# Optimization experiments

Hardware: AMD Instinct MI355X
Metric: run time of the kernel (lower is better)

The kernel has to match this reference:

```python
import jax, jax.numpy as jnp
import numpy as np

PROJ_EPS = 4e-3      # geoopt-style Poincare projection margin (float32)
MIN_NORM = 1e-15
ATANH_EPS = 1e-5     # clamp arg of arctanh away from 1
WEI_EPS = 1e-3       # self.eps buffer
P_EXP = 2.0          # self.p buffer


def _project(v, k):
    # Project onto Poincare ball of curvature -k: clip norm to (1-eps)/sqrt(k).
    # k has shape (1,H,1,1), v has shape (B,H,T,D).
    maxnorm = (1.0 - PROJ_EPS) / jnp.sqrt(k)
    norm = jnp.sqrt(jnp.clip(jnp.sum(v * v, axis=-1, keepdims=True), MIN_NORM))
    return jnp.where(norm > maxnorm, v / norm * maxnorm, v)


def setup_inputs() -> dict:
    key = jax.random.key(0)
    k1, k2, k3, k4 = jax.random.split(key, 4)
    B, T, C, H = 4, 1024, 768, 12
    x = jax.random.normal(k1, (B, T, C), dtype=jnp.float32)
    Wqkv = jax.random.normal(k2, (3 * C, C), dtype=jnp.float32) * (1.0 / np.sqrt(C))
    Wproj = jax.random.normal(k3, (C, C), dtype=jnp.float32) * (1.0 / np.sqrt(C))
    # learnable per-head curvature, init ~ exp(randn)*curvature (must be > 0)
    kcurv = jax.random.uniform(k4, (1, H, 1, 1), dtype=jnp.float32, minval=0.5, maxval=1.5)
    return {"x": x, "Wqkv": Wqkv, "Wproj": Wproj, "kcurv": kcurv}


def reference(x, Wqkv, Wproj, kcurv):
    B, T, C = x.shape
    H = kcurv.shape[1]
    D = C // H

    qkv = x @ Wqkv.T                                  # (B,T,3C)
    q, kx, v = jnp.split(qkv, 3, axis=-1)

    def to_heads(t):
        return t.reshape(B, T, H, D).transpose(0, 2, 1, 3)  # (B,H,T,D)

    q, kx, v = to_heads(q), to_heads(kx), to_heads(v)

    qp = _project(q, kcurv)
    kp = _project(kx, kcurv)

    # Poincare distance d(x,y) = (2/sqrt(k)) * artanh(sqrt(k)*||(-x) mobius+ y||).
    # mobius_add(-x,y) = (-(1-2k<x,y>+k|y|^2) x + (1-k|x|^2) y) / (1-2k<x,y>+k^2|x|^2|y|^2)
    # => ||num||^2 = A^2|x|^2 + Bc^2|y|^2 - 2*A*Bc*<x,y>, avoiding (B,H,T,T,D) tensors.
    x2 = jnp.sum(qp * qp, axis=-1)                    # (B,H,T)
    y2 = jnp.sum(kp * kp, axis=-1)                    # (B,H,T)
    xy = jnp.einsum('bhid,bhjd->bhij', qp, kp)        # (B,H,T,T)

    kc = kcurv                                        # (1,H,1,1) broadcasts to (B,H,T,T)
    x2i = x2[..., :, None]                            # (B,H,T,1)
    y2j = y2[..., None, :]                            # (B,H,1,T)

    A = 1.0 - 2.0 * kc * xy + kc * y2j
    Bc = 1.0 - kc * x2i
    num2 = A * A * x2i + Bc * Bc * y2j - 2.0 * A * Bc * xy
    denom = 1.0 - 2.0 * kc * xy + (kc * kc) * x2i * y2j
    madd_norm = jnp.sqrt(jnp.clip(num2, MIN_NORM)) / jnp.clip(denom, MIN_NORM)

    sk = jnp.sqrt(kc)
    dist = (2.0 / sk) * jnp.arctanh(jnp.clip(sk * madd_norm, 0.0, 1.0 - ATANH_EPS))

    wei = 1.0 / (WEI_EPS + dist ** P_EXP)             # (B,H,T,T)
    causal = jnp.tril(jnp.ones((T, T), dtype=bool))
    wei = jnp.where(causal, wei, 0.0)
    wei = wei / jnp.sum(wei, axis=-1, keepdims=True)

    y = jnp.einsum('bhij,bhjd->bhid', wei, v)         # (B,H,T,D)
    y = y.transpose(0, 2, 1, 3).reshape(B, T, C)
    return y @ Wproj.T
```

## Files before the change

### kernel.cpp

```cpp
#include <hip/hip_runtime.h>
#include <hip/hip_bf16.h>
#include <math.h>

#define PROJ_EPSF 0.004f
#define MIN_NORMF 1e-15f
#define ATANH_EPSF 1e-5f
#define WEI_EPSF 1e-3f
#define LN2F 0.69314718055994531f

#define TT 1024
#define CC 768
#define HH 12
#define BBATCH 4

typedef unsigned long long ull;
typedef __attribute__((ext_vector_type(4))) float f32x4;
typedef __attribute__((ext_vector_type(8))) short bf16x8;

#define MFMA(a, b, c) __builtin_amdgcn_mfma_f32_16x16x32_bf16(a, b, c, 0, 0, 0)

static __device__ __forceinline__ uint cvtpk(float a, float b) {
    uint r;
    asm("v_cvt_pk_bf16_f32 %0, %1, %2" : "=v"(r) : "v"(a), "v"(b));
    return r;
}
static __device__ __forceinline__ ushort f2bf(float f) {
    uint u = __float_as_uint(f);
    u += 0x7fffu + ((u >> 16) & 1u);
    return (ushort)(u >> 16);
}
static __device__ __forceinline__ float bf2f(ushort h) {
    return __uint_as_float(((uint)h) << 16);
}
static __device__ __forceinline__ void split4(const float4& f, ull& hp, ull& lp) {
    uint h01 = cvtpk(f.x, f.y), h23 = cvtpk(f.z, f.w);
    float r0 = f.x - __uint_as_float(h01 << 16);
    float r1 = f.y - __uint_as_float(h01 & 0xffff0000u);
    float r2 = f.z - __uint_as_float(h23 << 16);
    float r3 = f.w - __uint_as_float(h23 & 0xffff0000u);
    uint l01 = cvtpk(r0, r1), l23 = cvtpk(r2, r3);
    hp = ((ull)h23 << 32) | h01;
    lp = ((ull)l23 << 32) | l01;
}
union pk16 { bf16x8 v; ull u[2]; };
static __device__ __forceinline__ void gl_lds16(const void* g, void* l) {
    __builtin_amdgcn_global_load_lds(
        (const __attribute__((address_space(1))) unsigned int*)g,
        (__attribute__((address_space(3))) unsigned int*)l, 16, 0, 0);
}

__global__ __launch_bounds__(256) void wprep(const float* __restrict__ W,
                                             ushort* __restrict__ Wh,
                                             ushort* __restrict__ Wl, int n4) {
    int i = blockIdx.x * 256 + threadIdx.x;
    if (i < n4) {
        float4 f = ((const float4*)W)[i];
        ull hp, lp;
        split4(f, hp, lp);
        ((ull*)Wh)[i] = hp;
        ((ull*)Wl)[i] = lp;
    }
}

__global__ __launch_bounds__(256) void gemm_qkv(
        const float* __restrict__ x, const ushort* __restrict__ Wh,
        const ushort* __restrict__ Wl, const float* __restrict__ kcurv,
        ushort* __restrict__ qh, ushort* __restrict__ ql,
        ushort* __restrict__ kh, ushort* __restrict__ kl,
        ushort* __restrict__ vT, float* __restrict__ x2g,
        float* __restrict__ y2g) {
    __shared__ ushort Ah[2][64 * 64], Al[2][64 * 64], Bh[2][64 * 64], Bl[2][64 * 64];
    const int tid = threadIdx.x, lane = tid & 63, wv = tid >> 6;
    const int wr = wv >> 1, wc = wv & 1, lr = lane & 15, lg = lane >> 4;
    const int m0 = blockIdx.x * 128, n0 = blockIdx.y * 128;
    const bool isV = (n0 >= 2 * CC);

    const int arow = tid >> 1, akh = tid & 1;
    const float* Ap = x + (size_t)(m0 + arow) * CC + akh * 16;
    const int ap_ = arow >> 1;
    const int ag0 = 4 * (arow & 1) + 2 * akh;
    const int aoff0 = ap_ * 128 + ((ag0 ^ (ap_ & 7)) << 4);
    const int aoff1 = ap_ * 128 + (((ag0 + 1) ^ (ap_ & 7)) << 4);
    const int c0 = 2 * wv, c1 = 2 * wv + 1;
    const int p0 = 8 * c0 + (lane >> 3), q0 = (lane & 7) ^ (p0 & 7);
    const int p1 = 8 * c1 + (lane >> 3), q1 = (lane & 7) ^ (p1 & 7);
    const size_t bs0 = (size_t)(n0 + 2 * p0 + (q0 >> 2)) * CC + (q0 & 3) * 8;
    const size_t bs1 = (size_t)(n0 + 2 * p1 + (q1 >> 2)) * CC + (q1 & 3) * 8;
    const int goff = (((4 * (lr & 1) + lg) ^ ((lr >> 1) & 7)) << 4);
    const int pa = wr * 32 + (lr >> 1);
    const int pb = wc * 32 + (lr >> 1);

    f32x4 acc[4][4] = {};
    float4 av[4];

#define STAGE_B(BUF, KK)                                                          \
    gl_lds16(Wh + bs0 + (KK), (char*)Bh[BUF] + c0 * 1024);                        \
    gl_lds16(Wh + bs1 + (KK), (char*)Bh[BUF] + c1 * 1024);                        \
    if (!isV) {                                                                   \
        gl_lds16(Wl + bs0 + (KK), (char*)Bl[BUF] + c0 * 1024);                    \
        gl_lds16(Wl + bs1 + (KK), (char*)Bl[BUF] + c1 * 1024);                    \
    }
#define SPLIT_A(BUF)                                                              \
    {                                                                             \
        pk16 h_, l_;                                                              \
        split4(av[0], h_.u[0], l_.u[0]);                                          \
        split4(av[1], h_.u[1], l_.u[1]);                                          \
        *(bf16x8*)((char*)Ah[BUF] + aoff0) = h_.v;                                \
        if (!isV) *(bf16x8*)((char*)Al[BUF] + aoff0) = l_.v;                      \
        split4(av[2], h_.u[0], l_.u[0]);                                          \
        split4(av[3], h_.u[1], l_.u[1]);                                          \
        *(bf16x8*)((char*)Ah[BUF] + aoff1) = h_.v;                                \
        if (!isV) *(bf16x8*)((char*)Al[BUF] + aoff1) = l_.v;                      \
    }
#define LOAD_A(KK)                                                                \
    { _Pragma("unroll") for (int q = 0; q < 4; ++q)                               \
        av[q] = *(const float4*)(Ap + (KK) + 4 * q); }

    LOAD_A(0)
    STAGE_B(0, 0)
    SPLIT_A(0)
    LOAD_A(32)
    asm volatile("s_waitcnt vmcnt(4) lgkmcnt(0)" ::: "memory");
    __builtin_amdgcn_s_barrier();
    __builtin_amdgcn_sched_barrier(0);

    int cur = 0;
    for (int kk = 0; kk < CC; kk += 32) {
        const bool notLast = (kk + 32 < CC);
        if (notLast) {
            STAGE_B(cur ^ 1, kk + 32)
            SPLIT_A(cur ^ 1)
            if (kk + 64 < CC) LOAD_A(kk + 64)
            __builtin_amdgcn_sched_barrier(0);
        }
        if (!isV) {
            bf16x8 a_h[4], a_l[4];
#pragma unroll
            for (int m = 0; m < 4; ++m) {
                const int off = (pa + m * 8) * 128 + goff;
                a_h[m] = *(const bf16x8*)((char*)Ah[cur] + off);
                a_l[m] = *(const bf16x8*)((char*)Al[cur] + off);
            }
#pragma unroll
            for (int n = 0; n < 4; ++n) {
                const int off = (pb + n * 8) * 128 + goff;
                bf16x8 b_h = *(const bf16x8*)((char*)Bh[cur] + off);
                bf16x8 b_l = *(const bf16x8*)((char*)Bl[cur] + off);
#pragma unroll
                for (int m = 0; m < 4; ++m) {
                    acc[m][n] = MFMA(a_h[m], b_h, acc[m][n]);
                    acc[m][n] = MFMA(a_h[m], b_l, acc[m][n]);
                    acc[m][n] = MFMA(a_l[m], b_h, acc[m][n]);
                }
            }
        } else {
            bf16x8 a_h[4], b_h[4];
#pragma unroll
            for (int m = 0; m < 4; ++m)
                a_h[m] = *(const bf16x8*)((char*)Ah[cur] + (pa + m * 8) * 128 + goff);
#pragma unroll
            for (int n = 0; n < 4; ++n)
                b_h[n] = *(const bf16x8*)((char*)Bh[cur] + (pb + n * 8) * 128 + goff);
#pragma unroll
            for (int n = 0; n < 4; ++n)
#pragma unroll
                for (int m = 0; m < 4; ++m)
                    acc[n][m] = MFMA(b_h[n], a_h[m], acc[n][m]);
        }
        if (notLast) {
            if (kk + 64 < CC)
                asm volatile("s_waitcnt vmcnt(4) lgkmcnt(0)" ::: "memory");
            else
                asm volatile("s_waitcnt vmcnt(0) lgkmcnt(0)" ::: "memory");
            __builtin_amdgcn_s_barrier();
            __builtin_amdgcn_sched_barrier(0);
        }
        cur ^= 1;
    }
#undef STAGE_B
#undef SPLIT_A
#undef LOAD_A

    if (isV) {
        const int hd = (n0 - 2 * CC) / 64 + wc;
#pragma unroll
        for (int n = 0; n < 4; ++n)
#pragma unroll
            for (int m = 0; m < 4; ++m)
#pragma unroll
                for (int r = 0; r < 4; ++r) {
                    const int dl = n * 16 + lg * 4 + r;
                    const int tok = m0 + wr * 64 + m * 16 + lr;
                    vT[(size_t)(hd * 64 + dl) * 4096 + tok] = f2bf(acc[n][m][r]);
                }
    } else {
        const bool isQ = (n0 < CC);
        const int hd = (isQ ? n0 : n0 - CC) / 64 + wc;
        ushort* ph = isQ ? qh : kh;
        ushort* pl = isQ ? ql : kl;
        float* sg = isQ ? x2g : y2g;
        const float kcv = kcurv[hd];
        const float mxn = (1.0f - PROJ_EPSF) / sqrtf(kcv);
        const float mxn2 = mxn * mxn;
#pragma unroll
        for (int m = 0; m < 4; ++m)
#pragma unroll
            for (int r = 0; r < 4; ++r) {
                float s = 0.f;
#pragma unroll
                for (int n = 0; n < 4; ++n) s = fmaf(acc[m][n][r], acc[m][n][r], s);
                s += __shfl_xor(s, 1);
                s += __shfl_xor(s, 2);
                s += __shfl_xor(s, 4);
                s += __shfl_xor(s, 8);
                float scale = 1.0f, x2v = s;
                if (s > mxn2) {
                    scale = mxn * __builtin_amdgcn_rcpf(sqrtf(s));
                    x2v = s * scale * scale;
                }
                const int tok = m0 + wr * 64 + m * 16 + lg * 4 + r;
                const size_t rowb = (size_t)tok * CC + (isQ ? n0 : n0 - CC) + wc * 64;
#pragma unroll
                for (int n = 0; n < 4; ++n) {
                    const float v = acc[m][n][r] * scale;
                    const ushort hb = f2bf(v);
                    ph[rowb + n * 16 + lr] = hb;
                    pl[rowb + n * 16 + lr] = f2bf(v - bf2f(hb));
                }
                if (lr == 0)
                    sg[(size_t)((tok >> 10) * HH + hd) * TT + (tok & 1023)] = x2v;
            }
    }
}

__global__ __launch_bounds__(256) void hyp_attn(
        const ushort* __restrict__ qh, const ushort* __restrict__ ql,
        const ushort* __restrict__ kh, const ushort* __restrict__ kl,
        const ushort* __restrict__ vT, const float* __restrict__ x2g,
        const float* __restrict__ y2g, const float* __restrict__ kcurv,
        ushort* __restrict__ yh, ushort* __restrict__ yl) {
    const int ib = (int)blockIdx.x;
    const int xcd = ib & 7, t = ib >> 3;
    const int tcr = t / 6;
    const int which = t - tcr * 6;
    const int g64 = 15 - tcr;
    const int bh = which * 8 + xcd;
    const int b = bh / HH, h = bh - b * HH;
    const int tid = threadIdx.x, lane = tid & 63, wv = tid >> 6;
    const int lr = lane & 15, lg = lane >> 4;
    const int rg = g64 * 4 + wv;
    const int rgq = g64;

    __shared__ char ldsK[2][16384];
    __shared__ char ldsV[8192];
    __shared__ ushort wtb[4][16 * 72];
    ushort* wtw = wtb[wv];

    const float kc = kcurv[h];
    const float sk = sqrtf(kc);
    const float distc = LN2F / sk;
    const float d2c = distc * distc;
    const float twokc = 2.0f * kc;
    const float cA = 1.0f - ATANH_EPSF;

    const size_t qrb = (size_t)(b * TT + rg * 16 + lr) * CC + h * 64 + lg * 8;
    const bf16x8 qH0 = *(const bf16x8*)(qh + qrb), qH1 = *(const bf16x8*)(qh + qrb + 32);
    const bf16x8 qL0 = *(const bf16x8*)(ql + qrb), qL1 = *(const bf16x8*)(ql + qrb + 32);
    const float4 x2v = *(const float4*)&x2g[(size_t)bh * TT + rg * 16 + lg * 4];
    const float x2a[4] = { x2v.x, x2v.y, x2v.z, x2v.w };
    float kx2[4], Bc[4], Bc2[4];
#pragma unroll
    for (int r = 0; r < 4; ++r) {
        kx2[r] = kc * x2a[r];
        Bc[r] = 1.0f - kx2[r];
        Bc2[r] = Bc[r] * Bc[r];
    }

    const int srow8 = lane >> 3;
    const int sgrp = (lane & 7) ^ (srow8 & 7);
    const int so0 = ((lg ^ (lr & 7)) << 4);
    const int so1 = (((4 + lg) ^ (lr & 7)) << 4);
    const int lro = lr << 7;

#define STAGE_K(BUF, J0)                                                          \
    { _Pragma("unroll") for (int c4 = 0; c4 < 2; ++c4) {                          \
        const int c = wv * 2 + c4;                                                \
        const size_t gsrc = (size_t)(b * TT + (J0) + c * 8 + srow8) * CC + h * 64 + sgrp * 8; \
        gl_lds16(kh + gsrc, (char*)(BUF) + c * 1024);                             \
        gl_lds16(kl + gsrc, (char*)(BUF) + 8192 + c * 1024);                      \
    } }
#define STAGE_V(J0)                                                               \
    { _Pragma("unroll") for (int c4 = 0; c4 < 2; ++c4) {                          \
        const int c = wv * 2 + c4;                                                \
        gl_lds16(vT + (size_t)(h * 64 + c * 8 + srow8) * 4096 + b * TT + (J0) + sgrp * 8, \
                 ldsV + c * 1024);                                                \
    } }

#define TRANSF(NN, SA, Y2R)                                                        \
    {                                                                              \
        const float ky2 = kc * (Y2R);                                              \
        const float p1 = 1.0f + ky2;                                               \
        const int jg = j0 + NN * 16 + lr;                                          \
        _Pragma("unroll") for (int r = 0; r < 4; ++r) {                            \
            const float xy = SA[r];                                                \
            const float t2 = twokc * xy;                                           \
            const float Aa = p1 - t2;                                              \
            const float dn = fmaxf(fmaf(kx2[r], ky2, 1.0f) - t2, MIN_NORMF);       \
            const float ABxy = Aa * (Bc[r] * xy);                                  \
            const float c1 = fmaf(Bc2[r], (Y2R), -2.0f * ABxy);                    \
            const float num2 = fmaf(Aa * Aa, x2a[r], c1);                          \
            const float s = sqrtf(fmaxf(num2, MIN_NORMF));                         \
            const float sm = fminf(sk * s, cA * dn);                               \
            const float L = __builtin_amdgcn_logf((dn + sm) *                      \
                                __builtin_amdgcn_rcpf(dn - sm));                   \
            float w = __builtin_amdgcn_rcpf(fmaf(L * L, d2c, WEI_EPSF));           \
            if (mk && (jg > rg * 16 + lg * 4 + r)) w = 0.0f;                       \
            wtw[(lg * 4 + r) * 72 + NN * 16 + lr] = f2bf(w);                       \
            wsum[r] += w;                                                          \
        }                                                                          \
    }

    f32x4 pv[4] = {};
    float wsum[4] = {};

    STAGE_K(ldsK[0], 0)

    int cur = 0;
    for (int jt = 0; jt <= rgq; ++jt) {
        const int j0 = jt * 64;
        const bool mk = (jt == rgq);
        STAGE_V(j0)
        if (jt < rgq) {
            STAGE_K(ldsK[cur ^ 1], j0 + 64)
            asm volatile("s_waitcnt vmcnt(6)" ::: "memory");
        } else {
            asm volatile("s_waitcnt vmcnt(2)" ::: "memory");
        }
        __builtin_amdgcn_s_barrier();
        __builtin_amdgcn_sched_barrier(0);
        const size_t y2b = (size_t)bh * TT + j0 + lr;
        const float y2n[4] = { y2g[y2b], y2g[y2b + 16], y2g[y2b + 32], y2g[y2b + 48] };
        __builtin_amdgcn_s_setprio(1);
        f32x4 sacc[4] = {};
#pragma unroll
        for (int n = 0; n < 4; ++n) {
            const char* p = ldsK[cur] + n * 2048 + lro;
            bf16x8 h0 = *(const bf16x8*)(p + so0);
            bf16x8 h1 = *(const bf16x8*)(p + so1);
            bf16x8 l0 = *(const bf16x8*)(p + 8192 + so0);
            bf16x8 l1 = *(const bf16x8*)(p + 8192 + so1);
            sacc[n] = MFMA(qH0, h0, sacc[n]);
            sacc[n] = MFMA(qH0, l0, sacc[n]);
            sacc[n] = MFMA(qL0, h0, sacc[n]);
            sacc[n] = MFMA(qH1, h1, sacc[n]);
            sacc[n] = MFMA(qH1, l1, sacc[n]);
            sacc[n] = MFMA(qL1, h1, sacc[n]);
        }
        TRANSF(0, sacc[0], y2n[0])
        TRANSF(1, sacc[1], y2n[1])
        TRANSF(2, sacc[2], y2n[2])
        TRANSF(3, sacc[3], y2n[3])
        __builtin_amdgcn_s_setprio(0);
        if (jt < rgq)
            asm volatile("s_waitcnt vmcnt(4)" ::: "memory");
        else
            asm volatile("s_waitcnt vmcnt(0)" ::: "memory");
        __builtin_amdgcn_s_barrier();
        __builtin_amdgcn_sched_barrier(0);
        __builtin_amdgcn_s_setprio(1);
        bf16x8 pw0 = *(const bf16x8*)&wtw[lr * 72 + lg * 8];
        bf16x8 pw1 = *(const bf16x8*)&wtw[lr * 72 + 32 + lg * 8];
#pragma unroll
        for (int n = 0; n < 4; ++n) {
            const char* p = ldsV + n * 2048 + lro;
            bf16x8 v0 = *(const bf16x8*)(p + so0);
            bf16x8 v1 = *(const bf16x8*)(p + so1);
            pv[n] = MFMA(pw0, v0, pv[n]);
            pv[n] = MFMA(pw1, v1, pv[n]);
        }
        __builtin_amdgcn_s_setprio(0);
        __builtin_amdgcn_s_barrier();
        cur ^= 1;
    }

    float den[4];
#pragma unroll
    for (int r = 0; r < 4; ++r) {
        float s = wsum[r];
        s += __shfl_xor(s, 1);
        s += __shfl_xor(s, 2);
        s += __shfl_xor(s, 4);
        s += __shfl_xor(s, 8);
        den[r] = s;
    }
#pragma unroll
    for (int r = 0; r < 4; ++r) {
        const float iv = __builtin_amdgcn_rcpf(den[r]);
        const size_t rowb = (size_t)(b * TT + rg * 16 + lg * 4 + r) * CC + h * 64;
#pragma unroll
        for (int n = 0; n < 4; ++n) {
            const float val = pv[n][r] * iv;
            const ushort hb = f2bf(val);
            yh[rowb + n * 16 + lr] = hb;
            yl[rowb + n * 16 + lr] = f2bf(val - bf2f(hb));
        }
    }
#undef TRANSF
#undef STAGE_K
#undef STAGE_V
}

__global__ __launch_bounds__(256) void gemm_out(const ushort* __restrict__ Ahp,
                                                const ushort* __restrict__ Alp,
                                                const ushort* __restrict__ Wh,
                                                const ushort* __restrict__ Wl,
                                                float* __restrict__ C) {
    __shared__ ushort Ah[2][32 * 64], Al[2][32 * 64], Bh[2][32 * 64], Bl[2][32 * 64];
    const int tid = threadIdx.x, lane = tid & 63, wv = tid >> 6;
    const int wr = wv >> 1, wc = wv & 1, lr = lane & 15, lg = lane >> 4;
    const int m0 = blockIdx.x * 64, n0 = blockIdx.y * 64;

    const int sp = 8 * wv + (lane >> 3);
    const int sg = (lane & 7) ^ (sp & 7);
    const int srow = 2 * sp + (sg >> 2);
    const int scol = (sg & 3) * 8;
    const size_t asrc = (size_t)(m0 + srow) * CC + scol;
    const size_t bsrc = (size_t)(n0 + srow) * CC + scol;
    const int goff = (((4 * (lr & 1) + lg) ^ ((lr >> 1) & 7)) << 4);
    const int pa = wr * 16 + (lr >> 1);
    const int pb = wc * 16 + (lr >> 1);

    f32x4 acc[2][2] = {};

#define STAGE_O(BUF, KK)                                                          \
    gl_lds16(Ahp + asrc + (KK), (char*)Ah[BUF] + wv * 1024);                      \
    gl_lds16(Alp + asrc + (KK), (char*)Al[BUF] + wv * 1024);                      \
    gl_lds16(Wh + bsrc + (KK), (char*)Bh[BUF] + wv * 1024);                       \
    gl_lds16(Wl + bsrc + (KK), (char*)Bl[BUF] + wv * 1024);

    STAGE_O(0, 0)
    int cur = 0;
    for (int kk = 0; kk < CC; kk += 32) {
        if (kk + 32 < CC) {
            STAGE_O(cur ^ 1, kk + 32)
            asm volatile("s_waitcnt vmcnt(4)" ::: "memory");
        } else {
            asm volatile("s_waitcnt vmcnt(0)" ::: "memory");
        }
        __builtin_amdgcn_s_barrier();
        __builtin_amdgcn_sched_barrier(0);
        bf16x8 a_h[2], a_l[2];
#pragma unroll
        for (int m = 0; m < 2; ++m) {
            const int off = (pa + m * 8) * 128 + goff;
            a_h[m] = *(const bf16x8*)((char*)Ah[cur] + off);
            a_l[m] = *(const bf16x8*)((char*)Al[cur] + off);
        }
#pragma unroll
        for (int n = 0; n < 2; ++n) {
            const int off = (pb + n * 8) * 128 + goff;
            bf16x8 b_h = *(const bf16x8*)((char*)Bh[cur] + off);
            bf16x8 b_l = *(const bf16x8*)((char*)Bl[cur] + off);
#pragma unroll
            for (int m = 0; m < 2; ++m) {
                acc[m][n] = MFMA(a_h[m], b_h, acc[m][n]);
                acc[m][n] = MFMA(a_h[m], b_l, acc[m][n]);
                acc[m][n] = MFMA(a_l[m], b_h, acc[m][n]);
            }
        }
        __builtin_amdgcn_s_barrier();
        cur ^= 1;
    }
#undef STAGE_O
#pragma unroll
    for (int m = 0; m < 2; ++m)
#pragma unroll
        for (int n = 0; n < 2; ++n)
#pragma unroll
            for (int r = 0; r < 4; ++r)
                C[(size_t)(m0 + wr * 32 + m * 16 + lg * 4 + r) * CC + n0 + wc * 32 + n * 16 + lr] =
                    acc[m][n][r];
}

extern "C" void kernel_launch(void* const* d_in, const int* in_sizes, int n_in,
                              void* d_out, int out_size, void* d_ws, size_t ws_size,
                              hipStream_t stream) {
    const float* x     = (const float*)d_in[0];
    const float* Wqkv  = (const float*)d_in[1];
    const float* Wproj = (const float*)d_in[2];
    const float* kcurv = (const float*)d_in[3];
    float* out = (float*)d_out;

    const size_t PL = (size_t)4096 * CC;
    char* w = (char*)d_ws;
    ushort* Wqh = (ushort*)w;
    ushort* Wql = Wqh + (size_t)2304 * CC;
    ushort* yh  = (ushort*)w;
    ushort* yl  = yh + PL;
    ushort* qh  = (ushort*)(w + 2 * PL * 2);
    ushort* ql  = qh + PL;
    ushort* kh  = ql + PL;
    ushort* kl  = kh + PL;
    ushort* vT  = kl + PL;
    ushort* Wph = vT + PL;
    ushort* Wpl = Wph + (size_t)CC * CC;
    float* x2g  = (float*)(Wpl + (size_t)CC * CC);
    float* y2g  = x2g + 48 * TT;

    wprep<<<2304 * CC / 4 / 256, 256, 0, stream>>>(Wqkv, Wqh, Wql, 2304 * CC / 4);
    wprep<<<CC * CC / 4 / 256, 256, 0, stream>>>(Wproj, Wph, Wpl, CC * CC / 4);
    gemm_qkv<<<dim3(32, 18), 256, 0, stream>>>(x, Wqh, Wql, kcurv,
                                               qh, ql, kh, kl, vT, x2g, y2g);
    hyp_attn<<<768, 256, 0, stream>>>(qh, ql, kh, kl, vT, x2g, y2g, kcurv, yh, yl);
    gemm_out<<<dim3(64, 12), 256, 0, stream>>>(yh, yl, Wph, Wpl, out);
}
```

Baseline: 142.7 us.

## Widen attention blocks to 128 query rows and merge weight-prep launches

The attention kernel now runs 8 waves per block covering 128 query rows, so each staged K/V tile is shared by twice as many waves and each wave issues half as many global-to-LDS loads. Waves whose causal range has ended sit idle but still join the barriers until the block's last tile. The two weight-split launches are merged into one kernel. The aim is to cut K/V staging traffic and launch overhead, at the cost of causal imbalance inside blocks and lower per-block parallelism.

Measured after the change: 150.9 us. 5.8% more time.

```diff
diff --git a/kernel.cpp b/kernel.cpp
--- a/kernel.cpp
+++ b/kernel.cpp
@@ -49,16 +49,28 @@
         (__attribute__((address_space(3))) unsigned int*)l, 16, 0, 0);
 }
 
-__global__ __launch_bounds__(256) void wprep(const float* __restrict__ W,
-                                             ushort* __restrict__ Wh,
-                                             ushort* __restrict__ Wl, int n4) {
+__global__ __launch_bounds__(256) void wprep2(const float* __restrict__ Wq,
+                                              const float* __restrict__ Wp,
+                                              ushort* __restrict__ Wqh,
+                                              ushort* __restrict__ Wql,
+                                              ushort* __restrict__ Wph,
+                                              ushort* __restrict__ Wpl) {
+    const int n1 = 2304 * CC / 4;
+    const int n2 = CC * CC / 4;
     int i = blockIdx.x * 256 + threadIdx.x;
-    if (i < n4) {
-        float4 f = ((const float4*)W)[i];
+    if (i < n1) {
+        float4 f = ((const float4*)Wq)[i];
         ull hp, lp;
         split4(f, hp, lp);
-        ((ull*)Wh)[i] = hp;
-        ((ull*)Wl)[i] = lp;
+        ((ull*)Wqh)[i] = hp;
+        ((ull*)Wql)[i] = lp;
+    } else if (i < n1 + n2) {
+        int j = i - n1;
+        float4 f = ((const float4*)Wp)[j];
+        ull hp, lp;
+        split4(f, hp, lp);
+        ((ull*)Wph)[j] = hp;
+        ((ull*)Wpl)[j] = lp;
     }
 }
 
@@ -233,7 +245,7 @@
     }
 }
 
-__global__ __launch_bounds__(256) void hyp_attn(
+__global__ __launch_bounds__(512) void hyp_attn(
         const ushort* __restrict__ qh, const ushort* __restrict__ ql,
         const ushort* __restrict__ kh, const ushort* __restrict__ kl,
         const ushort* __restrict__ vT, const float* __restrict__ x2g,
@@ -241,19 +253,19 @@
         ushort* __restrict__ yh, ushort* __restrict__ yl) {
     const int ib = (int)blockIdx.x;
     const int xcd = ib & 7, t = ib >> 3;
-    const int tcr = t / 6;
-    const int which = t - tcr * 6;
-    const int g64 = 15 - tcr;
+    const int g128 = 7 - t / 6;
+    const int which = t % 6;
     const int bh = which * 8 + xcd;
     const int b = bh / HH, h = bh - b * HH;
     const int tid = threadIdx.x, lane = tid & 63, wv = tid >> 6;
     const int lr = lane & 15, lg = lane >> 4;
-    const int rg = g64 * 4 + wv;
-    const int rgq = g64;
+    const int rg = g128 * 8 + wv;
+    const int rgq = rg >> 2;
+    const int rgqMax = 2 * g128 + 1;
 
     __shared__ char ldsK[2][16384];
     __shared__ char ldsV[8192];
-    __shared__ ushort wtb[4][16 * 72];
+    __shared__ ushort wtb[8][16 * 72];
     ushort* wtw = wtb[wv];
 
     const float kc = kcurv[h];
@@ -283,18 +295,14 @@
     const int lro = lr << 7;
 
 #define STAGE_K(BUF, J0)                                                          \
-    { _Pragma("unroll") for (int c4 = 0; c4 < 2; ++c4) {                          \
-        const int c = wv * 2 + c4;                                                \
-        const size_t gsrc = (size_t)(b * TT + (J0) + c * 8 + srow8) * CC + h * 64 + sgrp * 8; \
-        gl_lds16(kh + gsrc, (char*)(BUF) + c * 1024);                             \
-        gl_lds16(kl + gsrc, (char*)(BUF) + 8192 + c * 1024);                      \
-    } }
+    {                                                                             \
+        const size_t gsrc = (size_t)(b * TT + (J0) + wv * 8 + srow8) * CC + h * 64 + sgrp * 8; \
+        gl_lds16(kh + gsrc, (char*)(BUF) + wv * 1024);                            \
+        gl_lds16(kl + gsrc, (char*)(BUF) + 8192 + wv * 1024);                     \
+    }
 #define STAGE_V(J0)                                                               \
-    { _Pragma("unroll") for (int c4 = 0; c4 < 2; ++c4) {                          \
-        const int c = wv * 2 + c4;                                                \
-        gl_lds16(vT + (size_t)(h * 64 + c * 8 + srow8) * 4096 + b * TT + (J0) + sgrp * 8, \
-                 ldsV + c * 1024);                                                \
-    } }
+    gl_lds16(vT + (size_t)(h * 64 + wv * 8 + srow8) * 4096 + b * TT + (J0) + sgrp * 8, \
+             ldsV + wv * 1024);
 
 #define TRANSF(NN, SA, Y2R)                                                        \
     {                                                                              \
@@ -326,59 +334,64 @@
     STAGE_K(ldsK[0], 0)
 
     int cur = 0;
-    for (int jt = 0; jt <= rgq; ++jt) {
+    for (int jt = 0; jt <= rgqMax; ++jt) {
         const int j0 = jt * 64;
+        const bool active = (jt <= rgq);
         const bool mk = (jt == rgq);
         STAGE_V(j0)
-        if (jt < rgq) {
+        if (jt < rgqMax) {
             STAGE_K(ldsK[cur ^ 1], j0 + 64)
-            asm volatile("s_waitcnt vmcnt(6)" ::: "memory");
+            asm volatile("s_waitcnt vmcnt(3)" ::: "memory");
         } else {
-            asm volatile("s_waitcnt vmcnt(2)" ::: "memory");
+            asm volatile("s_waitcnt vmcnt(1)" ::: "memory");
         }
         __builtin_amdgcn_s_barrier();
         __builtin_amdgcn_sched_barrier(0);
-        const size_t y2b = (size_t)bh * TT + j0 + lr;
-        const float y2n[4] = { y2g[y2b], y2g[y2b + 16], y2g[y2b + 32], y2g[y2b + 48] };
-        __builtin_amdgcn_s_setprio(1);
-        f32x4 sacc[4] = {};
-#pragma unroll
-        for (int n = 0; n < 4; ++n) {
-            const char* p = ldsK[cur] + n * 2048 + lro;
-            bf16x8 h0 = *(const bf16x8*)(p + so0);
-            bf16x8 h1 = *(const bf16x8*)(p + so1);
-            bf16x8 l0 = *(const bf16x8*)(p + 8192 + so0);
-            bf16x8 l1 = *(const bf16x8*)(p + 8192 + so1);
-            sacc[n] = MFMA(qH0, h0, sacc[n]);
-            sacc[n] = MFMA(qH0, l0, sacc[n]);
-            sacc[n] = MFMA(qL0, h0, sacc[n]);
-            sacc[n] = MFMA(qH1, h1, sacc[n]);
-            sacc[n] = MFMA(qH1, l1, sacc[n]);
-            sacc[n] = MFMA(qL1, h1, sacc[n]);
-        }
-        TRANSF(0, sacc[0], y2n[0])
-        TRANSF(1, sacc[1], y2n[1])
-        TRANSF(2, sacc[2], y2n[2])
-        TRANSF(3, sacc[3], y2n[3])
-        __builtin_amdgcn_s_setprio(0);
-        if (jt < rgq)
-            asm volatile("s_waitcnt vmcnt(4)" ::: "memory");
+        if (active) {
+            const size_t y2b = (size_t)bh * TT + j0 + lr;
+            const float y2n[4] = { y2g[y2b], y2g[y2b + 16], y2g[y2b + 32], y2g[y2b + 48] };
+            __builtin_amdgcn_s_setprio(1);
+            f32x4 sacc[4] = {};
+#pragma unroll
+            for (int n = 0; n < 4; ++n) {
+                const char* p = ldsK[cur] + n * 2048 + lro;
+                bf16x8 h0 = *(const bf16x8*)(p + so0);
+                bf16x8 h1 = *(const bf16x8*)(p + so1);
+                bf16x8 l0 = *(const bf16x8*)(p + 8192 + so0);
+                bf16x8 l1 = *(const bf16x8*)(p + 8192 + so1);
+                sacc[n] = MFMA(qH0, h0, sacc[n]);
+                sacc[n] = MFMA(qH0, l0, sacc[n]);
+                sacc[n] = MFMA(qL0, h0, sacc[n]);
+                sacc[n] = MFMA(qH1, h1, sacc[n]);
+                sacc[n] = MFMA(qH1, l1, sacc[n]);
+                sacc[n] = MFMA(qL1, h1, sacc[n]);
+            }
+            TRANSF(0, sacc[0], y2n[0])
+            TRANSF(1, sacc[1], y2n[1])
+            TRANSF(2, sacc[2], y2n[2])
+            TRANSF(3, sacc[3], y2n[3])
+            __builtin_amdgcn_s_setprio(0);
+        }
+        if (jt < rgqMax)
+            asm volatile("s_waitcnt vmcnt(2)" ::: "memory");
         else
             asm volatile("s_waitcnt vmcnt(0)" ::: "memory");
         __builtin_amdgcn_s_barrier();
         __builtin_amdgcn_sched_barrier(0);
-        __builtin_amdgcn_s_setprio(1);
-        bf16x8 pw0 = *(const bf16x8*)&wtw[lr * 72 + lg * 8];
-        bf16x8 pw1 = *(const bf16x8*)&wtw[lr * 72 + 32 + lg * 8];
-#pragma unroll
-        for (int n = 0; n < 4; ++n) {
-            const char* p = ldsV + n * 2048 + lro;
-            bf16x8 v0 = *(const bf16x8*)(p + so0);
-            bf16x8 v1 = *(const bf16x8*)(p + so1);
-            pv[n] = MFMA(pw0, v0, pv[n]);
-            pv[n] = MFMA(pw1, v1, pv[n]);
-        }
-        __builtin_amdgcn_s_setprio(0);
+        if (active) {
+            __builtin_amdgcn_s_setprio(1);
+            bf16x8 pw0 = *(const bf16x8*)&wtw[lr * 72 + lg * 8];
+            bf16x8 pw1 = *(const bf16x8*)&wtw[lr * 72 + 32 + lg * 8];
+#pragma unroll
+            for (int n = 0; n < 4; ++n) {
+                const char* p = ldsV + n * 2048 + lro;
+                bf16x8 v0 = *(const bf16x8*)(p + so0);
+                bf16x8 v1 = *(const bf16x8*)(p + so1);
+                pv[n] = MFMA(pw0, v0, pv[n]);
+                pv[n] = MFMA(pw1, v1, pv[n]);
+            }
+            __builtin_amdgcn_s_setprio(0);
+        }
         __builtin_amdgcn_s_barrier();
         cur ^= 1;
     }
@@ -507,10 +520,10 @@
     float* x2g  = (float*)(Wpl + (size_t)CC * CC);
     float* y2g  = x2g + 48 * TT;
 
-    wprep<<<2304 * CC / 4 / 256, 256, 0, stream>>>(Wqkv, Wqh, Wql, 2304 * CC / 4);
-    wprep<<<CC * CC / 4 / 256, 256, 0, stream>>>(Wproj, Wph, Wpl, CC * CC / 4);
+    const int nprep = (2304 * CC + CC * CC) / 4 / 256;
+    wprep2<<<nprep, 256, 0, stream>>>(Wqkv, Wproj, Wqh, Wql, Wph, Wpl);
     gemm_qkv<<<dim3(32, 18), 256, 0, stream>>>(x, Wqh, Wql, kcurv,
                                                qh, ql, kh, kl, vT, x2g, y2g);
-    hyp_attn<<<768, 256, 0, stream>>>(qh, ql, kh, kl, vT, x2g, y2g, kcurv, yh, yl);
+    hyp_attn<<<384, 512, 0, stream>>>(qh, ql, kh, kl, vT, x2g, y2g, kcurv, yh, yl);
     gemm_out<<<dim3(64, 12), 256, 0, stream>>>(yh, yl, Wph, Wpl, out);
 }
```
